# Optimization experiments

Measured on AMD Instinct MI355X. Metric: run time of the kernel, lower is better.

Reference implementation:

```python
import jax, jax.numpy as jnp
import numpy as np

IN_FEATURES = 256
OUT_FEATURES = 256
GRID_SIZE = 5
SPLINE_ORDER = 3
GRID_RANGE = (-1.0, 1.0)
LN_EPS = 1e-5


def _make_grid():
    h = (GRID_RANGE[1] - GRID_RANGE[0]) / GRID_SIZE
    n_knots = GRID_SIZE + 2 * SPLINE_ORDER + 1  # 12
    return jnp.linspace(GRID_RANGE[0] - h * SPLINE_ORDER,
                        GRID_RANGE[1] + h * SPLINE_ORDER,
                        n_knots, dtype=jnp.float32)


def setup_inputs() -> dict:
    key = jax.random.key(0)
    k1, k2, k3 = jax.random.split(key, 3)
    N = 65536
    # kaiming_uniform_(nonlinearity='linear'): bound = sqrt(3/fan_in)
    b1 = np.sqrt(3.0 / IN_FEATURES)
    fan_sp = IN_FEATURES * (GRID_SIZE + SPLINE_ORDER)
    b2 = np.sqrt(3.0 / fan_sp)
    return {
        "x": jax.random.normal(k1, (N, IN_FEATURES), dtype=jnp.float32),
        "grid": _make_grid(),
        "base_weight": jax.random.uniform(k2, (OUT_FEATURES, IN_FEATURES), jnp.float32, -b1, b1),
        "spline_weight": jax.random.uniform(k3, (OUT_FEATURES, IN_FEATURES, GRID_SIZE + SPLINE_ORDER), jnp.float32, -b2, b2),
        "ln_gamma": jnp.ones((OUT_FEATURES,), jnp.float32),
        "ln_beta": jnp.zeros((OUT_FEATURES,), jnp.float32),
        "prelu_a": jnp.full((1,), 0.25, jnp.float32),
    }


def reference(x, grid, base_weight, spline_weight, ln_gamma, ln_beta, prelu_a):
    # base branch: exact GELU then linear (matches nn.GELU() + F.linear)
    base_out = jnp.einsum('ni,oi->no', jax.nn.gelu(x, approximate=False), base_weight)

    # Cox-de Boor B-spline basis recursion. grid is identical per feature in
    # the original ([in, 12] expand of a 1D linspace) so we broadcast the 1D grid.
    xu = x[:, :, None]                                   # [N, in, 1]
    bases = ((xu >= grid[:-1]) & (xu < grid[1:])).astype(x.dtype)  # [N, in, 11]
    for k in range(1, SPLINE_ORDER + 1):
        left = grid[:-(k + 1)]
        right = grid[k:-1]
        delta = jnp.where(right == left, jnp.ones_like(right), right - left)
        bases = ((xu - left) / delta * bases[:, :, :-1]
                 + (grid[k + 1:] - xu) / (grid[k + 1:] - grid[1:-k]) * bases[:, :, 1:])
    # bases: [N, in, grid_size + spline_order]

    spline_out = jnp.einsum('nig,oig->no', bases, spline_weight)

    y = base_out + spline_out
    mu = jnp.mean(y, axis=-1, keepdims=True)
    var = jnp.mean(jnp.square(y - mu), axis=-1, keepdims=True)
    y = (y - mu) * jax.lax.rsqrt(var + LN_EPS) * ln_gamma + ln_beta
    # PReLU with a single shared slope (nn.PReLU default)
    return jnp.where(y >= 0, y, prelu_a[0] * y)
```

## Files before the change

### kernel.cpp

```cpp
#include <hip/hip_runtime.h>
#include <hip/hip_bf16.h>
#include <math.h>
#include <stdint.h>

typedef __attribute__((ext_vector_type(8))) short short8;
typedef __attribute__((ext_vector_type(4))) float f32x4;
typedef __attribute__((ext_vector_type(16))) float f32x16;

#define BM 256
#define NKT 36
#define A_BYTES (BM * 128)
#define LDS_TOTAL (4 * A_BYTES)

__device__ __forceinline__ unsigned short f2bf(float f) {
    __bf16 h = (__bf16)f;
    return __builtin_bit_cast(unsigned short, h);
}

__device__ __forceinline__ float gelu_exact(float x) {
    return 0.5f * x * (1.0f + erff(x * 0.7071067811865475f));
}

__device__ __forceinline__ int swz(int row, int u) {
    return row * 128 + ((u ^ (row & 7)) << 4);
}

__global__ void kan_prep_w(const float* __restrict__ bw, const float* __restrict__ sw,
                           unsigned short* __restrict__ Wf) {
    int U = blockIdx.x * 256 + threadIdx.x;
    if (U >= NKT * 2048) return;
    int kt = U >> 11, rem = U & 2047;
    int wcq = rem >> 9, rem2 = rem & 511;
    int i = rem2 >> 6;
    int lane = rem2 & 63;
    int o = wcq * 64 + (i & 1) * 32 + (lane & 31);
    int k0 = kt * 64 + (i >> 1) * 16 + (lane >> 5) * 8;
    unsigned short pk[8];
#pragma unroll
    for (int e = 0; e < 8; ++e) {
        int kk = k0 + e;
        float v = (kk < 256) ? bw[o * 256 + kk] : sw[o * 2048 + (kk - 256)];
        pk[e] = f2bf(v);
    }
    *(short8*)(Wf + (size_t)U * 8) = *(short8*)pk;
}

__device__ __forceinline__ short8 spline_row(float xv) {
    float xi = (xv + 2.2f) * 2.5f;
    float fi = floorf(xi);
    float tt = xi - fi;
    float s1 = 1.0f - tt;
    float t2 = tt * tt, t3 = t2 * tt;
    float w0 = s1 * s1 * s1 * (1.0f / 6.0f);
    float w1 = 0.5f * t3 - t2 + (2.0f / 3.0f);
    float w2 = -0.5f * t3 + 0.5f * t2 + 0.5f * tt + (1.0f / 6.0f);
    float w3 = t3 * (1.0f / 6.0f);
    uint64_t Wp = (uint64_t)f2bf(w0) | ((uint64_t)f2bf(w1) << 16)
                | ((uint64_t)f2bf(w2) << 32) | ((uint64_t)f2bf(w3) << 48);
    int b = 16 * ((int)fi - 3);
    uint64_t L = (b >= 0 && b < 64) ? (Wp << b)
               : ((b < 0 && b > -64) ? (Wp >> (-b)) : 0ull);
    uint64_t H = (b >= 64 && b < 128) ? (Wp << (b - 64))
               : ((b > 0 && b < 64) ? (Wp >> (64 - b)) : 0ull);
    union { uint64_t q[2]; short8 v; } rr;
    rr.q[0] = L; rr.q[1] = H;
    return rr.v;
}

__global__ __launch_bounds__(512)
void kan_fused(
    const float* __restrict__ X, const unsigned short* __restrict__ Wf,
    const float* __restrict__ gamma, const float* __restrict__ beta,
    const float* __restrict__ prelu_a, float* __restrict__ OUT)
{
    extern __shared__ __align__(16) unsigned char lds[];

    const int t = threadIdx.x;
    const int row0 = blockIdx.x * BM;
    const int wid = t >> 6, lane = t & 63;
    const int wr = wid >> 2, wc = wid & 3;
    const int l31 = lane & 31, l5 = lane >> 5;
    const int srow = t >> 3, scol = t & 7;

    f32x16 acc[4][2];
#pragma unroll
    for (int mt = 0; mt < 4; ++mt)
#pragma unroll
        for (int nt = 0; nt < 2; ++nt)
#pragma unroll
            for (int e = 0; e < 16; ++e) acc[mt][nt][e] = 0.f;

    const unsigned short* wlane = Wf + ((size_t)wc * 512 + lane) * 8;
    short8 wv[8];

    auto w_load = [&](int kt) {
        const unsigned short* wsrc = wlane + (size_t)kt * 2048 * 8;
#pragma unroll
        for (int i = 0; i < 8; ++i)
            wv[i] = *(const short8*)(wsrc + i * 512);
    };
    auto gelu_stage = [&](int kt, unsigned char* D) {
#pragma unroll
        for (int rep = 0; rep < 4; ++rep) {
            const float* xp = X + (size_t)(row0 + srow + rep * 64) * 256 + kt * 64 + scol * 8;
            float4 v0 = *(const float4*)xp;
            float4 v1 = *(const float4*)(xp + 4);
            float vv[8] = {v0.x, v0.y, v0.z, v0.w, v1.x, v1.y, v1.z, v1.w};
            unsigned short pk[8];
#pragma unroll
            for (int jj = 0; jj < 8; ++jj) pk[jj] = f2bf(gelu_exact(vv[jj]));
            *(short8*)(D + swz(srow + rep * 64, scol)) = *(short8*)pk;
        }
    };
    auto spline_stage = [&](float (&xs)[4], unsigned char* D) {
#pragma unroll
        for (int rep = 0; rep < 4; ++rep)
            *(short8*)(D + swz(srow + rep * 64, scol)) = spline_row(xs[rep]);
    };
    auto mfma_tile = [&](unsigned char* B) {
        __builtin_amdgcn_s_setprio(1);
#pragma unroll
        for (int ks = 0; ks < 4; ++ks) {
            short8 af[4];
#pragma unroll
            for (int mt = 0; mt < 4; ++mt)
                af[mt] = *(const short8*)(B + swz(wr * 128 + mt * 32 + l31, ks * 2 + l5));
#pragma unroll
            for (int mt = 0; mt < 4; ++mt)
#pragma unroll
                for (int nt = 0; nt < 2; ++nt)
                    acc[mt][nt] = __builtin_amdgcn_mfma_f32_32x32x16_bf16(
                        af[mt], wv[ks * 2 + nt], acc[mt][nt], 0, 0, 0);
        }
        __builtin_amdgcn_s_setprio(0);
    };

    w_load(0);
    gelu_stage(0, lds);
    gelu_stage(1, lds + A_BYTES);
    asm volatile("s_waitcnt lgkmcnt(0)\n\ts_barrier" ::: "memory");

    for (int j = 0; j < NKT / 2; ++j) {
        const int ka = 2 * j, kb = ka + 1;
        unsigned char* Ba = lds + (ka & 3) * A_BYTES;
        unsigned char* Bb = lds + (kb & 3) * A_BYTES;
        unsigned char* Sa = lds + ((ka + 2) & 3) * A_BYTES;
        unsigned char* Sb = lds + ((ka + 3) & 3) * A_BYTES;
        const bool stg = (ka + 2 < NKT);
        const bool gA = (ka + 2 < 4), gB = (ka + 3 < 4);

        float xsA[4], xsB[4];
        if (stg && !gA) {
            const int ibA = (ka + 2 - 4) * 8;
#pragma unroll
            for (int rep = 0; rep < 4; ++rep)
                xsA[rep] = X[(size_t)(row0 + srow + rep * 64) * 256 + ibA + scol];
        }
        if (stg && !gB) {
            const int ibB = (ka + 3 - 4) * 8;
#pragma unroll
            for (int rep = 0; rep < 4; ++rep)
                xsB[rep] = X[(size_t)(row0 + srow + rep * 64) * 256 + ibB + scol];
        }

        if ((wid & 1) == 0) {
            mfma_tile(Ba);
            w_load(kb);
            if (stg) { if (gA) gelu_stage(ka + 2, Sa); else spline_stage(xsA, Sa); }
            mfma_tile(Bb);
            if (stg) w_load(ka + 2);
            if (stg) { if (gB) gelu_stage(ka + 3, Sb); else spline_stage(xsB, Sb); }
        } else {
            if (stg) { if (gA) gelu_stage(ka + 2, Sa); else spline_stage(xsA, Sa); }
            mfma_tile(Ba);
            w_load(kb);
            if (stg) { if (gB) gelu_stage(ka + 3, Sb); else spline_stage(xsB, Sb); }
            mfma_tile(Bb);
            if (stg) w_load(ka + 2);
        }

        asm volatile("s_waitcnt lgkmcnt(0)\n\ts_barrier" ::: "memory");
    }

    float* stats = (float*)lds;
#pragma unroll
    for (int mt = 0; mt < 4; ++mt) {
#pragma unroll
        for (int r = 0; r < 16; ++r) {
            float v0 = acc[mt][0][r], v1 = acc[mt][1][r];
            float s = v0 + v1, s2 = v0 * v0 + v1 * v1;
#pragma unroll
            for (int msk = 1; msk < 32; msk <<= 1) {
                s  += __shfl_xor(s,  msk, 64);
                s2 += __shfl_xor(s2, msk, 64);
            }
            int row_local = (r & 3) + 8 * (r >> 2) + 4 * l5;
            if (l31 == row_local) {
                int row = wr * 128 + mt * 32 + row_local;
                stats[row * 8 + wc]     = s;
                stats[row * 8 + 4 + wc] = s2;
            }
        }
    }
    __syncthreads();

    const float apr = prelu_a[0];
    float gv[2], bv[2];
#pragma unroll
    for (int nt = 0; nt < 2; ++nt) {
        int col = wc * 64 + nt * 32 + l31;
        gv[nt] = gamma[col]; bv[nt] = beta[col];
    }
#pragma unroll
    for (int mt = 0; mt < 4; ++mt) {
#pragma unroll
        for (int r = 0; r < 16; ++r) {
            int row = wr * 128 + mt * 32 + (r & 3) + 8 * (r >> 2) + 4 * l5;
            f32x4 sv = *(const f32x4*)(stats + row * 8);
            f32x4 qv = *(const f32x4*)(stats + row * 8 + 4);
            float mu  = (sv[0] + sv[1] + sv[2] + sv[3]) * (1.0f / 256.0f);
            float ex2 = (qv[0] + qv[1] + qv[2] + qv[3]) * (1.0f / 256.0f);
            float rs = rsqrtf(ex2 - mu * mu + 1e-5f);
            float* op = OUT + (size_t)(row0 + row) * 256;
#pragma unroll
            for (int nt = 0; nt < 2; ++nt) {
                int col = wc * 64 + nt * 32 + l31;
                float y = (acc[mt][nt][r] - mu) * rs * gv[nt] + bv[nt];
                op[col] = (y >= 0.f) ? y : apr * y;
            }
        }
    }
}

extern "C" void kernel_launch(void* const* d_in, const int* in_sizes, int n_in,
                              void* d_out, int out_size, void* d_ws, size_t ws_size,
                              hipStream_t stream) {
    const float* x  = (const float*)d_in[0];
    const float* bw = (const float*)d_in[2];
    const float* sw = (const float*)d_in[3];
    const float* g  = (const float*)d_in[4];
    const float* be = (const float*)d_in[5];
    const float* pa = (const float*)d_in[6];
    float* out = (float*)d_out;
    unsigned short* Wf = (unsigned short*)d_ws;

    hipFuncSetAttribute((const void*)kan_fused,
                        hipFuncAttributeMaxDynamicSharedMemorySize, LDS_TOTAL);

    const int Nrows = in_sizes[0] / 256;
    kan_prep_w<<<(NKT * 2048 + 255) / 256, 256, 0, stream>>>(bw, sw, Wf);
    kan_fused<<<Nrows / BM, 512, LDS_TOTAL, stream>>>(x, Wf, g, be, pa, out);
}
```

Baseline: 125.2 us.

## Use column-major LDS A-tile layout with per-row thread staging

Replaces the XOR-swizzled row-major A tile in LDS with a layout of 16-byte column chunks, each strided by 4096 bytes. Each thread now owns one row and four column chunks. The spline stage loads four x values with a single float4 instead of four scalar loads, and the GELU stage loads 32 contiguous floats per thread. The aim is fewer, wider global loads and simpler LDS addressing. The risk is uncoalesced global access, since adjacent threads now touch different rows 1KB apart, and possible LDS bank conflicts without the swizzle.

```diff
diff --git a/kernel.cpp b/kernel.cpp
--- a/kernel.cpp
+++ b/kernel.cpp
@@ -21,9 +21,6 @@
     return 0.5f * x * (1.0f + erff(x * 0.7071067811865475f));
 }
 
-__device__ __forceinline__ int swz(int row, int u) {
-    return row * 128 + ((u ^ (row & 7)) << 4);
-}
 
 __global__ void kan_prep_w(const float* __restrict__ bw, const float* __restrict__ sw,
                            unsigned short* __restrict__ Wf) {
@@ -80,7 +77,7 @@
     const int wid = t >> 6, lane = t & 63;
     const int wr = wid >> 2, wc = wid & 3;
     const int l31 = lane & 31, l5 = lane >> 5;
-    const int srow = t >> 3, scol = t & 7;
+    const int sr = t & 255, su = (t >> 8) * 4;
 
     f32x16 acc[4][2];
 #pragma unroll
@@ -100,22 +97,27 @@
             wv[i] = *(const short8*)(wsrc + i * 512);
     };
     auto gelu_stage = [&](int kt, unsigned char* D) {
-#pragma unroll
-        for (int rep = 0; rep < 4; ++rep) {
-            const float* xp = X + (size_t)(row0 + srow + rep * 64) * 256 + kt * 64 + scol * 8;
-            float4 v0 = *(const float4*)xp;
-            float4 v1 = *(const float4*)(xp + 4);
-            float vv[8] = {v0.x, v0.y, v0.z, v0.w, v1.x, v1.y, v1.z, v1.w};
+        const float* xp = X + (size_t)(row0 + sr) * 256 + kt * 64 + su * 8;
+        float v[32];
+#pragma unroll
+        for (int j = 0; j < 8; ++j) {
+            float4 t4 = *(const float4*)(xp + j * 4);
+            v[j * 4 + 0] = t4.x; v[j * 4 + 1] = t4.y;
+            v[j * 4 + 2] = t4.z; v[j * 4 + 3] = t4.w;
+        }
+#pragma unroll
+        for (int j = 0; j < 4; ++j) {
             unsigned short pk[8];
 #pragma unroll
-            for (int jj = 0; jj < 8; ++jj) pk[jj] = f2bf(gelu_exact(vv[jj]));
-            *(short8*)(D + swz(srow + rep * 64, scol)) = *(short8*)pk;
-        }
-    };
-    auto spline_stage = [&](float (&xs)[4], unsigned char* D) {
-#pragma unroll
-        for (int rep = 0; rep < 4; ++rep)
-            *(short8*)(D + swz(srow + rep * 64, scol)) = spline_row(xs[rep]);
+            for (int e = 0; e < 8; ++e) pk[e] = f2bf(gelu_exact(v[j * 8 + e]));
+            *(short8*)(D + (su + j) * 4096 + sr * 16) = *(short8*)pk;
+        }
+    };
+    auto spline_stage = [&](float4 xs, unsigned char* D) {
+        *(short8*)(D + (su + 0) * 4096 + sr * 16) = spline_row(xs.x);
+        *(short8*)(D + (su + 1) * 4096 + sr * 16) = spline_row(xs.y);
+        *(short8*)(D + (su + 2) * 4096 + sr * 16) = spline_row(xs.z);
+        *(short8*)(D + (su + 3) * 4096 + sr * 16) = spline_row(xs.w);
     };
     auto mfma_tile = [&](unsigned char* B) {
         __builtin_amdgcn_s_setprio(1);
@@ -124,7 +126,8 @@
             short8 af[4];
 #pragma unroll
             for (int mt = 0; mt < 4; ++mt)
-                af[mt] = *(const short8*)(B + swz(wr * 128 + mt * 32 + l31, ks * 2 + l5));
+                af[mt] = *(const short8*)(B + (ks * 2 + l5) * 4096
+                                          + (wr * 128 + mt * 32 + l31) * 16);
 #pragma unroll
             for (int mt = 0; mt < 4; ++mt)
 #pragma unroll
@@ -149,19 +152,11 @@
         const bool stg = (ka + 2 < NKT);
         const bool gA = (ka + 2 < 4), gB = (ka + 3 < 4);
 
-        float xsA[4], xsB[4];
-        if (stg && !gA) {
-            const int ibA = (ka + 2 - 4) * 8;
-#pragma unroll
-            for (int rep = 0; rep < 4; ++rep)
-                xsA[rep] = X[(size_t)(row0 + srow + rep * 64) * 256 + ibA + scol];
-        }
-        if (stg && !gB) {
-            const int ibB = (ka + 3 - 4) * 8;
-#pragma unroll
-            for (int rep = 0; rep < 4; ++rep)
-                xsB[rep] = X[(size_t)(row0 + srow + rep * 64) * 256 + ibB + scol];
-        }
+        float4 xsA, xsB;
+        if (stg && !gA)
+            xsA = *(const float4*)(X + (size_t)(row0 + sr) * 256 + (ka + 2 - 4) * 8 + su);
+        if (stg && !gB)
+            xsB = *(const float4*)(X + (size_t)(row0 + sr) * 256 + (ka + 3 - 4) * 8 + su);
 
         if ((wid & 1) == 0) {
             mfma_tile(Ba);
```

Measured after the change: 128.4 us. +2.5%, slower.
